# Optimization experiments

Measured on AMD Instinct MI355X. Metric: run time of the kernel, lower is better.

The kernel has to match this reference:

```python
import jax, jax.numpy as jnp
import numpy as np

DIM = 512
NUM_HEADS = 8
POS_DIM = 2
K_CLUSTERS = 256
M_PTS = 256


def setup_inputs() -> dict:
    key = jax.random.key(0)
    ks = jax.random.split(key, 9)
    pos = jax.random.uniform(ks[0], (K_CLUSTERS, M_PTS, POS_DIM), dtype=jnp.float32)
    feat = jax.random.normal(ks[1], (K_CLUSTERS, M_PTS, DIM), dtype=jnp.float32)
    mask = jax.random.randint(ks[2], (K_CLUSTERS, M_PTS, 1), 0, 2, dtype=jnp.int32)
    s = 0.02
    qkv_w = jax.random.normal(ks[3], (DIM, 3 * DIM), dtype=jnp.float32) * s
    qkv_b = jnp.zeros((3 * DIM,), dtype=jnp.float32)
    pos_w = jax.random.normal(ks[4], (POS_DIM, NUM_HEADS), dtype=jnp.float32) * s
    pos_b = jnp.zeros((NUM_HEADS,), dtype=jnp.float32)
    proj_w = jax.random.normal(ks[5], (DIM, DIM), dtype=jnp.float32) * s
    proj_b = jnp.zeros((DIM,), dtype=jnp.float32)
    return {"pos": pos, "feat": feat, "qkv_w": qkv_w, "qkv_b": qkv_b,
            "pos_w": pos_w, "pos_b": pos_b, "proj_w": proj_w, "proj_b": proj_b,
            "mask": mask}


def reference(pos, feat, qkv_w, qkv_b, pos_w, pos_b, proj_w, proj_b, mask):
    k_, m, c = feat.shape
    H = pos_w.shape[1]
    hd = c // H
    scale = hd ** -0.5

    # qkv projection -> (3, k, H, m, hd)
    qkv = (feat @ qkv_w + qkv_b).reshape(k_, m, 3, H, hd).transpose(2, 0, 3, 1, 4)
    q, k, v = qkv[0], qkv[1], qkv[2]

    attn = jnp.einsum('khid,khjd->khij', q * scale, k)  # k,H,m,m

    # normalize each coordinate by its global max over all clusters/points
    pos_n = pos / jnp.max(pos, axis=(0, 1), keepdims=True)
    # rel_pos[k,a,b,d] = pos[k,b,d] - pos[k,a,d]
    rel_pos = pos_n[:, None, :, :] - pos_n[:, :, None, :]  # k,m,m,d
    pos_bias = rel_pos @ pos_w + pos_b                      # k,m,m,H
    attn = attn + pos_bias.transpose(0, 3, 1, 2)            # k,H,m,m

    # mask: k,m,1 -> additive bias over key dim
    maskf = mask[:, :, 0].astype(attn.dtype)                # k,m
    attn = attn + ((1.0 - maskf) * -100.0)[:, None, None, :]

    attn = jax.nn.softmax(attn, axis=-1)
    x = jnp.einsum('khij,khjd->khid', attn, v)              # k,H,m,hd
    x = x.transpose(0, 2, 1, 3).reshape(k_, m, c)
    x = x @ proj_w + proj_b
    return x
```

## Files before the change

kernel.cpp:

```cpp
#include <hip/hip_runtime.h>
#include <stdint.h>

typedef short bf16x8 __attribute__((ext_vector_type(8)));
typedef float f32x4 __attribute__((ext_vector_type(4)));
typedef unsigned short u16x4 __attribute__((ext_vector_type(4)));
typedef unsigned short ushort_t;

__device__ __forceinline__ float bf2f(unsigned short u) {
    union { unsigned int i; float f; } v; v.i = ((unsigned int)u) << 16; return v.f;
}
__device__ __forceinline__ unsigned short f2bf(float f) {
    union { float f; unsigned int i; } v; v.f = f;
    unsigned int r = (v.i + 0x7FFFu + ((v.i >> 16) & 1u)) >> 16;
    return (unsigned short)r;
}

__device__ __forceinline__ void gload_lds16(const void* g, void* l) {
    __builtin_amdgcn_global_load_lds(
        (const __attribute__((address_space(1))) void*)g,
        (__attribute__((address_space(3))) void*)l, 16, 0, 0);
}

template <bool F32> struct LD;
template <> struct LD<false> {
    static __device__ __forceinline__ float s(const void* p, size_t i) {
        return bf2f(((const ushort_t*)p)[i]);
    }
    static __device__ __forceinline__ bf16x8 v8(const void* p, size_t i) {
        return *reinterpret_cast<const bf16x8*>((const ushort_t*)p + i);
    }
};
template <> struct LD<true> {
    static __device__ __forceinline__ float s(const void* p, size_t i) {
        return ((const float*)p)[i];
    }
    static __device__ __forceinline__ bf16x8 v8(const void* p, size_t i) {
        const float* f = (const float*)p + i;
        float4 a = *reinterpret_cast<const float4*>(f);
        float4 b = *reinterpret_cast<const float4*>(f + 4);
        bf16x8 r;
        r[0] = (short)f2bf(a.x); r[1] = (short)f2bf(a.y);
        r[2] = (short)f2bf(a.z); r[3] = (short)f2bf(a.w);
        r[4] = (short)f2bf(b.x); r[5] = (short)f2bf(b.y);
        r[6] = (short)f2bf(b.z); r[7] = (short)f2bf(b.w);
        return r;
    }
};

__global__ __launch_bounds__(64) void kprobe(const ushort_t* __restrict__ pos, int* __restrict__ dt) {
    float v = bf2f(pos[2 * threadIdx.x]);
    bool sane = (v >= 0.0f) && (v <= 1.0f);
    unsigned long long b = __ballot(sane);
    if (threadIdx.x == 0) dt[0] = (b == ~0ULL) ? 1 : 0;
}

template <bool F32>
static __device__ __forceinline__ void kpos_body(const void* pos, int* pmax, float* s0, float* s1) {
    int p = blockIdx.x * 256 + threadIdx.x;
    s0[threadIdx.x] = LD<F32>::s(pos, 2 * (size_t)p);
    s1[threadIdx.x] = LD<F32>::s(pos, 2 * (size_t)p + 1);
    __syncthreads();
    for (int off = 128; off > 0; off >>= 1) {
        if (threadIdx.x < (unsigned)off) {
            s0[threadIdx.x] = fmaxf(s0[threadIdx.x], s0[threadIdx.x + off]);
            s1[threadIdx.x] = fmaxf(s1[threadIdx.x], s1[threadIdx.x + off]);
        }
        __syncthreads();
    }
    if (threadIdx.x == 0) {
        atomicMax(&pmax[0], __float_as_int(s0[0]));
        atomicMax(&pmax[1], __float_as_int(s1[0]));
    }
}
__global__ __launch_bounds__(256) void kpos_max(const int* __restrict__ dt, const void* __restrict__ pos,
                                                int* __restrict__ pmax) {
    __shared__ float s0[256], s1[256];
    if (dt[0]) kpos_body<false>(pos, pmax, s0, s1);
    else       kpos_body<true>(pos, pmax, s0, s1);
}

template <bool F32>
static __device__ __forceinline__ void ktb_body(const void* pos, const void* pos_w, const int* mask,
                                                const int* pmax, float* tb) {
    int p = blockIdx.x * 256 + threadIdx.x;
    float inv0 = 1.0f / __int_as_float(pmax[0]);
    float inv1 = 1.0f / __int_as_float(pmax[1]);
    float x0 = LD<F32>::s(pos, 2 * (size_t)p) * inv0;
    float x1 = LD<F32>::s(pos, 2 * (size_t)p + 1) * inv1;
    float mterm = mask[p] ? 0.0f : -100.0f;
#pragma unroll
    for (int h = 0; h < 8; h++)
        tb[p * 8 + h] = x0 * LD<F32>::s(pos_w, h) + x1 * LD<F32>::s(pos_w, 8 + h) + mterm;
}
__global__ __launch_bounds__(256) void ktb(const int* __restrict__ dt, const void* __restrict__ pos,
                                           const void* __restrict__ pos_w, const int* __restrict__ mask,
                                           const int* __restrict__ pmax, float* __restrict__ tb) {
    if (dt[0]) ktb_body<false>(pos, pos_w, mask, pmax, tb);
    else       ktb_body<true>(pos, pos_w, mask, pmax, tb);
}

__global__ __launch_bounds__(256) void kbias(const int* __restrict__ dt, const void* __restrict__ qkv_b,
                                             const void* __restrict__ proj_b,
                                             float* __restrict__ qb, float* __restrict__ pb) {
    int i = blockIdx.x * 256 + threadIdx.x;
    if (dt[0]) {
        if (i < 1536) qb[i] = bf2f(((const ushort_t*)qkv_b)[i]);
        if (i < 512)  pb[i] = bf2f(((const ushort_t*)proj_b)[i]);
    } else {
        if (i < 1536) qb[i] = ((const float*)qkv_b)[i];
        if (i < 512)  pb[i] = ((const float*)proj_b)[i];
    }
}

template <bool F32>
static __device__ __forceinline__ void kfeat_body(const void* feat, ushort_t* featb) {
    for (size_t t = (size_t)blockIdx.x * 256 + threadIdx.x; t < 4194304; t += (size_t)gridDim.x * 256) {
        *reinterpret_cast<bf16x8*>(featb + t * 8) = LD<F32>::v8(feat, t * 8);
    }
}
__global__ __launch_bounds__(256) void kfeat(const int* __restrict__ dt, const void* __restrict__ feat,
                                             ushort_t* __restrict__ featb) {
    if (dt[0]) kfeat_body<false>(feat, featb);
    else       kfeat_body<true>(feat, featb);
}

template <bool F32>
static __device__ __forceinline__ void ktrans_body(const void* src, ushort_t* dst, int R, int C,
                                                   ushort_t* tile ) {
    int nbc = C >> 6;
    int rb = (blockIdx.x / nbc) << 6;
    int cb = (blockIdx.x % nbc) << 6;
    for (int i = threadIdx.x; i < 4096; i += 256) {
        int r = i >> 6, c = i & 63;
        tile[r * 65 + c] = f2bf(LD<F32>::s(src, (size_t)(rb + r) * C + cb + c));
    }
    __syncthreads();
    for (int i = threadIdx.x; i < 4096; i += 256) {
        int rr = i & 63, cc = i >> 6;
        dst[(size_t)(cb + cc) * R + rb + rr] = tile[rr * 65 + cc];
    }
}
__global__ __launch_bounds__(256) void ktrans(const int* __restrict__ dt, const void* __restrict__ src,
                                              ushort_t* __restrict__ dst, int R, int C) {
    __shared__ ushort_t tile[64 * 65];
    if (dt[0]) ktrans_body<false>(src, dst, R, C, tile);
    else       ktrans_body<true>(src, dst, R, C, tile);
}

template <bool F32>
static __device__ __forceinline__ void kattn_body(const void* feat, const ushort_t* qkv_wt,
                                                  const float* qb, const float* tb, ushort_t* xout,
                                                  ushort_t* smem) {
    const int tid = threadIdx.x;
    const int lane = tid & 63;
    const int wave = tid >> 6;
    const int quad = lane >> 4;
    const int l15 = lane & 15;

    const int bx = blockIdx.x;
    const int xcd = bx & 7;
    const int jj = bx >> 3;
    const int rr = jj >> 5;
    const int ss = jj & 31;
    const int kc = xcd * 32 + rr * 4 + (ss >> 3);
    const int h = ss & 7;

    ushort_t* sQ  = smem;
    ushort_t* sK  = smem + 18432;
    ushort_t* sVt = smem + 36864;
    ushort_t* sP  = smem + 53760;
    float*    stb = (float*)(smem + 72192);
    char*     stg = (char*)smem;

    if (tid < 256) stb[tid] = tb[(size_t)(kc * 256 + tid) * 8 + h];

    const int t0 = tid, t1 = tid + 512, t2 = tid + 1024;
    const int r0 = t0 >> 3, r1 = t1 >> 3, r2 = t2 >> 3;
    const ushort_t* g0 = qkv_wt + (size_t)((r0 >> 6) * 512 + h * 64 + (r0 & 63)) * 512 + (((t0 & 7) ^ (r0 & 7)) * 8);
    const ushort_t* g1 = qkv_wt + (size_t)((r1 >> 6) * 512 + h * 64 + (r1 & 63)) * 512 + (((t1 & 7) ^ (r1 & 7)) * 8);
    const ushort_t* g2 = qkv_wt + (size_t)((r2 >> 6) * 512 + h * 64 + (r2 & 63)) * 512 + (((t2 & 7) ^ (r2 & 7)) * 8);

    const int wrow = (wave >> 1) * 64;
    const int wcol = (wave & 1) * 96;

    f32x4 acc[4][6];
#pragma unroll
    for (int rt = 0; rt < 4; rt++)
#pragma unroll
        for (int ct = 0; ct < 6; ct++) {
            f32x4 z = {0.0f, 0.0f, 0.0f, 0.0f};
            acc[rt][ct] = z;
        }

    const size_t fbase = (size_t)(kc * 256) * 512;

    gload_lds16(g0, stg + t0 * 16);
    gload_lds16(g1, stg + t1 * 16);
    gload_lds16(g2, stg + t2 * 16);
    __syncthreads();

#pragma unroll 2
    for (int it = 0; it < 8; it++) {
        if (it < 7) {
            const int nb = ((it + 1) & 1) * 24576;
            gload_lds16(g0 + (it + 1) * 64, stg + nb + t0 * 16);
            gload_lds16(g1 + (it + 1) * 64, stg + nb + t1 * 16);
            gload_lds16(g2 + (it + 1) * 64, stg + nb + t2 * 16);
        }
        const int cbu = (it & 1) * 12288;
#pragma unroll
        for (int s = 0; s < 2; s++) {
            bf16x8 af[4];
#pragma unroll
            for (int rt = 0; rt < 4; rt++)
                af[rt] = LD<F32>::v8(
                    feat, fbase + (size_t)(wrow + rt * 16 + l15) * 512 + it * 64 + s * 32 + quad * 8);
            bf16x8 bw[6];
#pragma unroll
            for (int ct = 0; ct < 6; ct++) {
                const int rw = wcol + ct * 16 + l15;
                bw[ct] = *reinterpret_cast<const bf16x8*>(
                    smem + cbu + rw * 64 + (((s * 4 + quad) ^ (rw & 7)) * 8));
            }
#pragma unroll
            for (int ct = 0; ct < 6; ct++)
#pragma unroll
                for (int rt = 0; rt < 4; rt++)
                    acc[rt][ct] = __builtin_amdgcn_mfma_f32_16x16x32_bf16(af[rt], bw[ct], acc[rt][ct], 0, 0, 0);
        }
        __syncthreads();
    }

#pragma unroll
    for (int ct = 0; ct < 6; ct++) {
        const int lcb = wcol + ct * 16;
        const int mat = lcb >> 6;
        const int col = (lcb & 63) + l15;
        const float bias = qb[mat * 512 + h * 64 + col];
#pragma unroll
        for (int rt = 0; rt < 4; rt++) {
            const int m0 = wrow + rt * 16 + quad * 4;
            if (mat == 0) {
#pragma unroll
                for (int r = 0; r < 4; r++)
                    sQ[(m0 + r) * 72 + col] = f2bf((acc[rt][ct][r] + bias) * 0.125f);
            } else if (mat == 1) {
#pragma unroll
                for (int r = 0; r < 4; r++)
                    sK[(m0 + r) * 72 + col] = f2bf(acc[rt][ct][r] + bias);
            } else {
                u16x4 vp;
#pragma unroll
                for (int r = 0; r < 4; r++) vp[r] = f2bf(acc[rt][ct][r] + bias);
                *reinterpret_cast<u16x4*>(&sVt[col * 264 + m0]) = vp;
            }
        }
    }
    __syncthreads();

    bf16x8 aQ[2][2];
#pragma unroll
    for (int rt = 0; rt < 2; rt++)
#pragma unroll
        for (int s = 0; s < 2; s++)
            aQ[rt][s] = *reinterpret_cast<const bf16x8*>(
                &sQ[(wave * 32 + rt * 16 + l15) * 72 + s * 32 + quad * 8]);

    f32x4 accO[2][4];
    float rs[2][4];
#pragma unroll
    for (int rt = 0; rt < 2; rt++)
#pragma unroll
        for (int ct = 0; ct < 4; ct++) {
            f32x4 z = {0.0f, 0.0f, 0.0f, 0.0f};
            accO[rt][ct] = z;
            rs[rt][ct] = 0.0f;
        }

    ushort_t* sPw = sP + wave * (32 * 72);

    for (int jb = 0; jb < 4; jb++) {
        int kb = jb * 64;
        bf16x8 bK[4][2];
#pragma unroll
        for (int ctk = 0; ctk < 4; ctk++)
#pragma unroll
            for (int s = 0; s < 2; s++)
                bK[ctk][s] = *reinterpret_cast<const bf16x8*>(
                    &sK[(kb + ctk * 16 + l15) * 72 + s * 32 + quad * 8]);

#pragma unroll
        for (int ctk = 0; ctk < 4; ctk++) {
            float tcol = stb[kb + ctk * 16 + l15];
#pragma unroll
            for (int rt = 0; rt < 2; rt++) {
                f32x4 sa = {0.0f, 0.0f, 0.0f, 0.0f};
                sa = __builtin_amdgcn_mfma_f32_16x16x32_bf16(aQ[rt][0], bK[ctk][0], sa, 0, 0, 0);
                sa = __builtin_amdgcn_mfma_f32_16x16x32_bf16(aQ[rt][1], bK[ctk][1], sa, 0, 0, 0);
                int rl0 = rt * 16 + quad * 4;
#pragma unroll
                for (int r = 0; r < 4; r++) {
                    float pexp = __expf(sa[r] + tcol);
                    rs[rt][r] += pexp;
                    sPw[(rl0 + r) * 72 + ctk * 16 + l15] = f2bf(pexp);
                }
            }
        }

#pragma unroll
        for (int s = 0; s < 2; s++) {
            bf16x8 aP[2];
#pragma unroll
            for (int rt = 0; rt < 2; rt++)
                aP[rt] = *reinterpret_cast<const bf16x8*>(
                    &sPw[(rt * 16 + l15) * 72 + s * 32 + quad * 8]);
#pragma unroll
            for (int ct = 0; ct < 4; ct++) {
                bf16x8 bV = *reinterpret_cast<const bf16x8*>(
                    &sVt[(ct * 16 + l15) * 264 + kb + s * 32 + quad * 8]);
#pragma unroll
                for (int rt = 0; rt < 2; rt++)
                    accO[rt][ct] =
                        __builtin_amdgcn_mfma_f32_16x16x32_bf16(aP[rt], bV, accO[rt][ct], 0, 0, 0);
            }
        }
    }

    float inv_[2][4];
#pragma unroll
    for (int rt = 0; rt < 2; rt++)
#pragma unroll
        for (int r = 0; r < 4; r++) {
            float v = rs[rt][r];
            v += __shfl_xor(v, 1, 64);
            v += __shfl_xor(v, 2, 64);
            v += __shfl_xor(v, 4, 64);
            v += __shfl_xor(v, 8, 64);
            inv_[rt][r] = 1.0f / v;
        }

#pragma unroll
    for (int rt = 0; rt < 2; rt++)
#pragma unroll
        for (int ct = 0; ct < 4; ct++)
#pragma unroll
            for (int r = 0; r < 4; r++) {
                int m = wave * 32 + rt * 16 + quad * 4 + r;
                xout[((size_t)(kc * 256 + m)) * 512 + h * 64 + ct * 16 + l15] =
                    f2bf(accO[rt][ct][r] * inv_[rt][r]);
            }
}
__global__ __launch_bounds__(512, 2) void kattn_bf(const ushort_t* __restrict__ featb,
                                                   const ushort_t* __restrict__ qkv_wt,
                                                   const float* __restrict__ qb,
                                                   const float* __restrict__ tb, ushort_t* __restrict__ xout) {
    __shared__ ushort_t smem[72704];
    kattn_body<false>(featb, qkv_wt, qb, tb, xout, smem);
}
__global__ __launch_bounds__(512, 2) void kattn_dyn(const int* __restrict__ dt, const void* __restrict__ feat,
                                                    const ushort_t* __restrict__ qkv_wt,
                                                    const float* __restrict__ qb,
                                                    const float* __restrict__ tb, ushort_t* __restrict__ xout) {
    __shared__ ushort_t smem[72704];
    if (dt[0]) kattn_body<false>(feat, qkv_wt, qb, tb, xout, smem);
    else       kattn_body<true>(feat, qkv_wt, qb, tb, xout, smem);
}

template <bool F32>
static __device__ __forceinline__ void kproj_body(const ushort_t* x, const ushort_t* proj_wt,
                                                  const float* pb, void* out, ushort_t* sW) {
    const int tid = threadIdx.x;
    const int lane = tid & 63;
    const int wave = tid >> 6;
    const int quad = lane >> 4;
    const int l15 = lane & 15;
    const int bx = blockIdx.x;
    const int xcd = bx & 7;
    const int j = bx >> 3;
    const int rowb = (xcd * 32 + (j >> 2)) * 256;
    const int colb = (j & 3) * 128;
    const int rowg = (wave >> 1) * 64;
    const int colg = (wave & 1) * 64;
    char* stg = (char*)sW;

    const int t0 = tid, t1 = tid + 512;
    const int r0 = t0 >> 3, r1 = t1 >> 3;
    const ushort_t* g0 = proj_wt + (size_t)(colb + r0) * 512 + (((t0 & 7) ^ (r0 & 7)) * 8);
    const ushort_t* g1 = proj_wt + (size_t)(colb + r1) * 512 + (((t1 & 7) ^ (r1 & 7)) * 8);

    f32x4 acc[4][4];
#pragma unroll
    for (int rt = 0; rt < 4; rt++)
#pragma unroll
        for (int ct = 0; ct < 4; ct++) {
            f32x4 z = {0.0f, 0.0f, 0.0f, 0.0f};
            acc[rt][ct] = z;
        }

    gload_lds16(g0, stg + t0 * 16);
    gload_lds16(g1, stg + t1 * 16);
    __syncthreads();

#pragma unroll 2
    for (int it = 0; it < 8; it++) {
        if (it < 7) {
            const int nb = ((it + 1) & 1) * 16384;
            gload_lds16(g0 + (it + 1) * 64, stg + nb + t0 * 16);
            gload_lds16(g1 + (it + 1) * 64, stg + nb + t1 * 16);
        }
        const int cbu = (it & 1) * 8192;
#pragma unroll
        for (int s = 0; s < 2; s++) {
            bf16x8 af[4];
#pragma unroll
            for (int rt = 0; rt < 4; rt++) {
                int m = rowb + rowg + rt * 16 + l15;
                af[rt] = *reinterpret_cast<const bf16x8*>(
                    x + (size_t)m * 512 + it * 64 + s * 32 + quad * 8);
            }
            bf16x8 bw[4];
#pragma unroll
            for (int ct = 0; ct < 4; ct++) {
                const int rw = colg + ct * 16 + l15;
                bw[ct] = *reinterpret_cast<const bf16x8*>(
                    sW + cbu + rw * 64 + (((s * 4 + quad) ^ (rw & 7)) * 8));
            }
#pragma unroll
            for (int ct = 0; ct < 4; ct++)
#pragma unroll
                for (int rt = 0; rt < 4; rt++)
                    acc[rt][ct] = __builtin_amdgcn_mfma_f32_16x16x32_bf16(af[rt], bw[ct], acc[rt][ct], 0, 0, 0);
        }
        __syncthreads();
    }

#pragma unroll
    for (int ct = 0; ct < 4; ct++) {
        int n = colb + colg + ct * 16 + l15;
        float bias = pb[n];
#pragma unroll
        for (int rt = 0; rt < 4; rt++)
#pragma unroll
            for (int r = 0; r < 4; r++) {
                int m = rowb + rowg + rt * 16 + quad * 4 + r;
                float v = acc[rt][ct][r] + bias;
                if (F32) ((float*)out)[(size_t)m * 512 + n] = v;
                else     ((ushort_t*)out)[(size_t)m * 512 + n] = f2bf(v);
            }
    }
}
__global__ __launch_bounds__(512, 4) void kproj(const int* __restrict__ dt, const ushort_t* __restrict__ x,
                                                const ushort_t* __restrict__ proj_wt,
                                                const float* __restrict__ pb, void* __restrict__ out) {
    __shared__ ushort_t sW[16384];
    if (dt[0]) kproj_body<false>(x, proj_wt, pb, out, sW);
    else       kproj_body<true>(x, proj_wt, pb, out, sW);
}

extern "C" void kernel_launch(void* const* d_in, const int* in_sizes, int n_in,
                              void* d_out, int out_size, void* d_ws, size_t ws_size,
                              hipStream_t stream) {
    (void)in_sizes; (void)n_in; (void)out_size;
    const void* pos    = d_in[0];
    const void* feat   = d_in[1];
    const void* qkv_w  = d_in[2];
    const void* qkv_b  = d_in[3];
    const void* pos_w  = d_in[4];
    const void* proj_w = d_in[6];
    const void* proj_b = d_in[7];
    const int* mask    = (const int*)d_in[8];

    char* ws = (char*)d_ws;
    int* pmax         = (int*)ws;
    int* dtf          = (int*)ws + 2;
    float* qb         = (float*)(ws + 256);
    float* pb         = (float*)(ws + 256 + 6144);
    float* tb         = (float*)(ws + 16384);
    ushort_t* qkv_wt  = (ushort_t*)(ws + 16384 + 2097152);
    ushort_t* proj_wt = qkv_wt + 786432;
    ushort_t* x       = proj_wt + 262144;
    ushort_t* featb   = x + 33554432;
    const size_t NEED = 16384 + 2097152 + 1572864 + 524288 + 67108864 + 67108864;
    const bool big = ws_size >= NEED;

    (void)hipMemsetAsync(ws, 0, 16, stream);
    kprobe<<<1, 64, 0, stream>>>((const ushort_t*)pos, dtf);
    kpos_max<<<256, 256, 0, stream>>>(dtf, pos, pmax);
    ktb<<<256, 256, 0, stream>>>(dtf, pos, pos_w, mask, pmax, tb);
    kbias<<<6, 256, 0, stream>>>(dtf, qkv_b, proj_b, qb, pb);
    ktrans<<<192, 256, 0, stream>>>(dtf, qkv_w, qkv_wt, 512, 1536);
    ktrans<<<64, 256, 0, stream>>>(dtf, proj_w, proj_wt, 512, 512);
    if (big) {
        kfeat<<<2048, 256, 0, stream>>>(dtf, feat, featb);
        kattn_bf<<<2048, 512, 0, stream>>>(featb, qkv_wt, qb, tb, x);
    } else {
        kattn_dyn<<<2048, 512, 0, stream>>>(dtf, feat, qkv_wt, qb, tb, x);
    }
    kproj<<<1024, 512, 0, stream>>>(dtf, x, proj_wt, pb, d_out);
}
```

Before: 594.3 us.

## Merge preprocessing kernels into one launch and compute pos/mask bias inside attention

Replaces the probe, pos-max, bias, transpose and feature-conversion kernels with a single kprep kernel whose blocks are partitioned by index across those tasks. The per-point pos/mask bias table is no longer precomputed; the attention kernel now computes it from pos, pos_w, mask and the global max. The QKV weight staging in the attention GEMM changes from 64-wide swizzled chunks to 32-wide double-buffered chunks over 16 iterations, and LDS is split into separate arrays. This removes several launches and a workspace round trip, in exchange for more barriers per GEMM pass and possibly more LDS bank conflicts without the swizzle.

```diff
diff --git a/kernel.cpp b/kernel.cpp
--- a/kernel.cpp
+++ b/kernel.cpp
@@ -47,16 +47,26 @@
     }
 };
 
-__global__ __launch_bounds__(64) void kprobe(const ushort_t* __restrict__ pos, int* __restrict__ dt) {
-    float v = bf2f(pos[2 * threadIdx.x]);
-    bool sane = (v >= 0.0f) && (v <= 1.0f);
-    unsigned long long b = __ballot(sane);
-    if (threadIdx.x == 0) dt[0] = (b == ~0ULL) ? 1 : 0;
-}
-
 template <bool F32>
-static __device__ __forceinline__ void kpos_body(const void* pos, int* pmax, float* s0, float* s1) {
-    int p = blockIdx.x * 256 + threadIdx.x;
+static __device__ __forceinline__ void ktrans_body(const void* src, ushort_t* dst, int R, int C,
+                                                   ushort_t* tile , int bx) {
+    int nbc = C >> 6;
+    int rb = (bx / nbc) << 6;
+    int cb = (bx % nbc) << 6;
+    for (int i = threadIdx.x; i < 4096; i += 256) {
+        int r = i >> 6, c = i & 63;
+        tile[r * 65 + c] = f2bf(LD<F32>::s(src, (size_t)(rb + r) * C + cb + c));
+    }
+    __syncthreads();
+    for (int i = threadIdx.x; i < 4096; i += 256) {
+        int rr = i & 63, cc = i >> 6;
+        dst[(size_t)(cb + cc) * R + rb + rr] = tile[rr * 65 + cc];
+    }
+}
+
+template <bool F32>
+static __device__ __forceinline__ void kpos_body(const void* pos, int* pmax, float* s0, float* s1, int bx) {
+    int p = bx * 256 + threadIdx.x;
     s0[threadIdx.x] = LD<F32>::s(pos, 2 * (size_t)p);
     s1[threadIdx.x] = LD<F32>::s(pos, 2 * (size_t)p + 1);
     __syncthreads();
@@ -72,85 +82,72 @@
         atomicMax(&pmax[1], __float_as_int(s1[0]));
     }
 }
-__global__ __launch_bounds__(256) void kpos_max(const int* __restrict__ dt, const void* __restrict__ pos,
-                                                int* __restrict__ pmax) {
-    __shared__ float s0[256], s1[256];
-    if (dt[0]) kpos_body<false>(pos, pmax, s0, s1);
-    else       kpos_body<true>(pos, pmax, s0, s1);
-}
-
-template <bool F32>
-static __device__ __forceinline__ void ktb_body(const void* pos, const void* pos_w, const int* mask,
-                                                const int* pmax, float* tb) {
-    int p = blockIdx.x * 256 + threadIdx.x;
-    float inv0 = 1.0f / __int_as_float(pmax[0]);
-    float inv1 = 1.0f / __int_as_float(pmax[1]);
-    float x0 = LD<F32>::s(pos, 2 * (size_t)p) * inv0;
-    float x1 = LD<F32>::s(pos, 2 * (size_t)p + 1) * inv1;
-    float mterm = mask[p] ? 0.0f : -100.0f;
-#pragma unroll
-    for (int h = 0; h < 8; h++)
-        tb[p * 8 + h] = x0 * LD<F32>::s(pos_w, h) + x1 * LD<F32>::s(pos_w, 8 + h) + mterm;
-}
-__global__ __launch_bounds__(256) void ktb(const int* __restrict__ dt, const void* __restrict__ pos,
-                                           const void* __restrict__ pos_w, const int* __restrict__ mask,
-                                           const int* __restrict__ pmax, float* __restrict__ tb) {
-    if (dt[0]) ktb_body<false>(pos, pos_w, mask, pmax, tb);
-    else       ktb_body<true>(pos, pos_w, mask, pmax, tb);
-}
-
-__global__ __launch_bounds__(256) void kbias(const int* __restrict__ dt, const void* __restrict__ qkv_b,
-                                             const void* __restrict__ proj_b,
-                                             float* __restrict__ qb, float* __restrict__ pb) {
-    int i = blockIdx.x * 256 + threadIdx.x;
-    if (dt[0]) {
-        if (i < 1536) qb[i] = bf2f(((const ushort_t*)qkv_b)[i]);
-        if (i < 512)  pb[i] = bf2f(((const ushort_t*)proj_b)[i]);
+
+__global__ __launch_bounds__(256) void kprep(const void* __restrict__ pos, const void* __restrict__ feat,
+                                             const void* __restrict__ qkv_w, const void* __restrict__ proj_w,
+                                             const void* __restrict__ qkv_b, const void* __restrict__ proj_b,
+                                             int* __restrict__ pmax, int* __restrict__ dtf,
+                                             float* __restrict__ qb, float* __restrict__ pb,
+                                             ushort_t* __restrict__ featb,
+                                             ushort_t* __restrict__ qkv_wt, ushort_t* __restrict__ proj_wt) {
+    __shared__ char smem[8448];
+    __shared__ int sdt;
+    const int tid = threadIdx.x;
+    if (tid < 64) {
+        float v = bf2f(((const ushort_t*)pos)[2 * tid]);
+        bool sane = (v >= 0.0f) && (v <= 1.0f);
+        unsigned long long b = __ballot(sane);
+        if (tid == 0) sdt = (b == ~0ULL) ? 1 : 0;
+    }
+    __syncthreads();
+    const bool isbf = (sdt != 0);
+    const int bx = blockIdx.x;
+
+    if (bx < 192) {
+        ushort_t* tile = (ushort_t*)smem;
+        if (isbf) ktrans_body<false>(qkv_w, qkv_wt, 512, 1536, tile, bx);
+        else      ktrans_body<true>(qkv_w, qkv_wt, 512, 1536, tile, bx);
+    } else if (bx < 256) {
+        ushort_t* tile = (ushort_t*)smem;
+        if (isbf) ktrans_body<false>(proj_w, proj_wt, 512, 512, tile, bx - 192);
+        else      ktrans_body<true>(proj_w, proj_wt, 512, 512, tile, bx - 192);
+    } else if (bx < 512) {
+        float* s0 = (float*)smem;
+        float* s1 = s0 + 256;
+        if (isbf) kpos_body<false>(pos, pmax, s0, s1, bx - 256);
+        else      kpos_body<true>(pos, pmax, s0, s1, bx - 256);
+    } else if (bx == 512) {
+        if (tid == 0) dtf[0] = isbf ? 1 : 0;
+        for (int i = tid; i < 1536; i += 256)
+            qb[i] = isbf ? bf2f(((const ushort_t*)qkv_b)[i]) : ((const float*)qkv_b)[i];
+        for (int i = tid; i < 512; i += 256)
+            pb[i] = isbf ? bf2f(((const ushort_t*)proj_b)[i]) : ((const float*)proj_b)[i];
     } else {
-        if (i < 1536) qb[i] = ((const float*)qkv_b)[i];
-        if (i < 512)  pb[i] = ((const float*)proj_b)[i];
-    }
-}
-
-template <bool F32>
-static __device__ __forceinline__ void kfeat_body(const void* feat, ushort_t* featb) {
-    for (size_t t = (size_t)blockIdx.x * 256 + threadIdx.x; t < 4194304; t += (size_t)gridDim.x * 256) {
-        *reinterpret_cast<bf16x8*>(featb + t * 8) = LD<F32>::v8(feat, t * 8);
-    }
-}
-__global__ __launch_bounds__(256) void kfeat(const int* __restrict__ dt, const void* __restrict__ feat,
-                                             ushort_t* __restrict__ featb) {
-    if (dt[0]) kfeat_body<false>(feat, featb);
-    else       kfeat_body<true>(feat, featb);
-}
-
-template <bool F32>
-static __device__ __forceinline__ void ktrans_body(const void* src, ushort_t* dst, int R, int C,
-                                                   ushort_t* tile ) {
-    int nbc = C >> 6;
-    int rb = (blockIdx.x / nbc) << 6;
-    int cb = (blockIdx.x % nbc) << 6;
-    for (int i = threadIdx.x; i < 4096; i += 256) {
-        int r = i >> 6, c = i & 63;
-        tile[r * 65 + c] = f2bf(LD<F32>::s(src, (size_t)(rb + r) * C + cb + c));
-    }
-    __syncthreads();
-    for (int i = threadIdx.x; i < 4096; i += 256) {
-        int rr = i & 63, cc = i >> 6;
-        dst[(size_t)(cb + cc) * R + rb + rr] = tile[rr * 65 + cc];
-    }
-}
-__global__ __launch_bounds__(256) void ktrans(const int* __restrict__ dt, const void* __restrict__ src,
-                                              ushort_t* __restrict__ dst, int R, int C) {
-    __shared__ ushort_t tile[64 * 65];
-    if (dt[0]) ktrans_body<false>(src, dst, R, C, tile);
-    else       ktrans_body<true>(src, dst, R, C, tile);
+        const int fb = bx - 513;
+        if (isbf) {
+#pragma unroll
+            for (int i = 0; i < 8; i++) {
+                size_t t = (size_t)fb * 256 + tid + (size_t)i * 524288;
+                *reinterpret_cast<bf16x8*>(featb + t * 8) = LD<false>::v8(feat, t * 8);
+            }
+        } else {
+#pragma unroll
+            for (int i = 0; i < 8; i++) {
+                size_t t = (size_t)fb * 256 + tid + (size_t)i * 524288;
+                *reinterpret_cast<bf16x8*>(featb + t * 8) = LD<true>::v8(feat, t * 8);
+            }
+        }
+    }
 }
 
 template <bool F32>
 static __device__ __forceinline__ void kattn_body(const void* feat, const ushort_t* qkv_wt,
-                                                  const float* qb, const float* tb, ushort_t* xout,
-                                                  ushort_t* smem) {
+                                                  const float* qb,
+                                                  const void* pos, const void* pos_w,
+                                                  const int* mask, const int* pmax, int dtv,
+                                                  ushort_t* xout,
+                                                  ushort_t* sQ, ushort_t* sK, ushort_t* sVt,
+                                                  ushort_t* sP, float* stb) {
     const int tid = threadIdx.x;
     const int lane = tid & 63;
     const int wave = tid >> 6;
@@ -165,23 +162,41 @@
     const int kc = xcd * 32 + rr * 4 + (ss >> 3);
     const int h = ss & 7;
 
-    ushort_t* sQ  = smem;
-    ushort_t* sK  = smem + 18432;
-    ushort_t* sVt = smem + 36864;
-    ushort_t* sP  = smem + 53760;
-    float*    stb = (float*)(smem + 72192);
-    char*     stg = (char*)smem;
-
-    if (tid < 256) stb[tid] = tb[(size_t)(kc * 256 + tid) * 8 + h];
-
-    const int t0 = tid, t1 = tid + 512, t2 = tid + 1024;
-    const int r0 = t0 >> 3, r1 = t1 >> 3, r2 = t2 >> 3;
-    const ushort_t* g0 = qkv_wt + (size_t)((r0 >> 6) * 512 + h * 64 + (r0 & 63)) * 512 + (((t0 & 7) ^ (r0 & 7)) * 8);
-    const ushort_t* g1 = qkv_wt + (size_t)((r1 >> 6) * 512 + h * 64 + (r1 & 63)) * 512 + (((t1 & 7) ^ (r1 & 7)) * 8);
-    const ushort_t* g2 = qkv_wt + (size_t)((r2 >> 6) * 512 + h * 64 + (r2 & 63)) * 512 + (((t2 & 7) ^ (r2 & 7)) * 8);
+    if (tid < 256) {
+        const int p = kc * 256 + tid;
+        const float inv0 = 1.0f / __int_as_float(pmax[0]);
+        const float inv1 = 1.0f / __int_as_float(pmax[1]);
+        float x0, x1, w0, w1;
+        if (dtv) {
+            x0 = bf2f(((const ushort_t*)pos)[2 * (size_t)p]);
+            x1 = bf2f(((const ushort_t*)pos)[2 * (size_t)p + 1]);
+            w0 = bf2f(((const ushort_t*)pos_w)[h]);
+            w1 = bf2f(((const ushort_t*)pos_w)[8 + h]);
+        } else {
+            x0 = ((const float*)pos)[2 * (size_t)p];
+            x1 = ((const float*)pos)[2 * (size_t)p + 1];
+            w0 = ((const float*)pos_w)[h];
+            w1 = ((const float*)pos_w)[8 + h];
+        }
+        x0 *= inv0;
+        x1 *= inv1;
+        const float mterm = mask[p] ? 0.0f : -100.0f;
+        stb[tid] = x0 * w0 + x1 * w1 + mterm;
+    }
+
+    ushort_t* sW = sP;
+    char* ldsW = (char*)sW;
+
+    const int t1 = wave * 64 + lane;
+    const int t2 = 512 + t1;
+    const int lc1 = t1 >> 2, ch1 = t1 & 3;
+    const int lc2 = t2 >> 2, ch2 = t2 & 3;
+    const ushort_t* g1 = qkv_wt + (size_t)((lc1 >> 6) * 512 + h * 64 + (lc1 & 63)) * 512 + ch1 * 8;
+    const ushort_t* g2 = qkv_wt + (size_t)((lc2 >> 6) * 512 + h * 64 + (lc2 & 63)) * 512 + ch2 * 8;
 
     const int wrow = (wave >> 1) * 64;
     const int wcol = (wave & 1) * 96;
+    const int fcol = quad * 8;
 
     f32x4 acc[4][6];
 #pragma unroll
@@ -194,40 +209,31 @@
 
     const size_t fbase = (size_t)(kc * 256) * 512;
 
-    gload_lds16(g0, stg + t0 * 16);
-    gload_lds16(g1, stg + t1 * 16);
-    gload_lds16(g2, stg + t2 * 16);
+    gload_lds16(g1, ldsW + wave * 1024);
+    if (wave < 4) gload_lds16(g2, ldsW + 8192 + wave * 1024);
     __syncthreads();
 
 #pragma unroll 2
-    for (int it = 0; it < 8; it++) {
-        if (it < 7) {
-            const int nb = ((it + 1) & 1) * 24576;
-            gload_lds16(g0 + (it + 1) * 64, stg + nb + t0 * 16);
-            gload_lds16(g1 + (it + 1) * 64, stg + nb + t1 * 16);
-            gload_lds16(g2 + (it + 1) * 64, stg + nb + t2 * 16);
-        }
-        const int cbu = (it & 1) * 12288;
-#pragma unroll
-        for (int s = 0; s < 2; s++) {
-            bf16x8 af[4];
+    for (int c = 0; c < 16; c++) {
+        const int cb = (c & 1) * 6144;
+        const int nbB = ((c + 1) & 1) * 12288;
+        if (c < 15) {
+            gload_lds16(g1 + (c + 1) * 32, ldsW + nbB + wave * 1024);
+            if (wave < 4) gload_lds16(g2 + (c + 1) * 32, ldsW + nbB + 8192 + wave * 1024);
+        }
+        bf16x8 af[4];
+#pragma unroll
+        for (int rt = 0; rt < 4; rt++)
+            af[rt] = LD<F32>::v8(feat, fbase + (size_t)(wrow + rt * 16 + l15) * 512 + c * 32 + fcol);
+        bf16x8 bw[6];
+#pragma unroll
+        for (int ct = 0; ct < 6; ct++)
+            bw[ct] = *reinterpret_cast<const bf16x8*>(sW + cb + (wcol + ct * 16 + l15) * 32 + fcol);
+#pragma unroll
+        for (int ct = 0; ct < 6; ct++)
 #pragma unroll
             for (int rt = 0; rt < 4; rt++)
-                af[rt] = LD<F32>::v8(
-                    feat, fbase + (size_t)(wrow + rt * 16 + l15) * 512 + it * 64 + s * 32 + quad * 8);
-            bf16x8 bw[6];
-#pragma unroll
-            for (int ct = 0; ct < 6; ct++) {
-                const int rw = wcol + ct * 16 + l15;
-                bw[ct] = *reinterpret_cast<const bf16x8*>(
-                    smem + cbu + rw * 64 + (((s * 4 + quad) ^ (rw & 7)) * 8));
-            }
-#pragma unroll
-            for (int ct = 0; ct < 6; ct++)
-#pragma unroll
-                for (int rt = 0; rt < 4; rt++)
-                    acc[rt][ct] = __builtin_amdgcn_mfma_f32_16x16x32_bf16(af[rt], bw[ct], acc[rt][ct], 0, 0, 0);
-        }
+                acc[rt][ct] = __builtin_amdgcn_mfma_f32_16x16x32_bf16(af[rt], bw[ct], acc[rt][ct], 0, 0, 0);
         __syncthreads();
     }
 
@@ -353,17 +359,34 @@
 __global__ __launch_bounds__(512, 2) void kattn_bf(const ushort_t* __restrict__ featb,
                                                    const ushort_t* __restrict__ qkv_wt,
                                                    const float* __restrict__ qb,
-                                                   const float* __restrict__ tb, ushort_t* __restrict__ xout) {
-    __shared__ ushort_t smem[72704];
-    kattn_body<false>(featb, qkv_wt, qb, tb, xout, smem);
-}
-__global__ __launch_bounds__(512, 2) void kattn_dyn(const int* __restrict__ dt, const void* __restrict__ feat,
+                                                   const void* __restrict__ pos,
+                                                   const void* __restrict__ pos_w,
+                                                   const int* __restrict__ mask,
+                                                   const int* __restrict__ pmax,
+                                                   const int* __restrict__ dtf,
+                                                   ushort_t* __restrict__ xout) {
+    __shared__ ushort_t sQ[256 * 72];
+    __shared__ ushort_t sK[256 * 72];
+    __shared__ ushort_t sVt[64 * 264];
+    __shared__ ushort_t sP[8 * 32 * 72];
+    __shared__ float stb[256];
+    kattn_body<false>(featb, qkv_wt, qb, pos, pos_w, mask, pmax, dtf[0], xout, sQ, sK, sVt, sP, stb);
+}
+__global__ __launch_bounds__(512, 2) void kattn_dyn(const int* __restrict__ dtf, const void* __restrict__ feat,
                                                     const ushort_t* __restrict__ qkv_wt,
                                                     const float* __restrict__ qb,
-                                                    const float* __restrict__ tb, ushort_t* __restrict__ xout) {
-    __shared__ ushort_t smem[72704];
-    if (dt[0]) kattn_body<false>(feat, qkv_wt, qb, tb, xout, smem);
-    else       kattn_body<true>(feat, qkv_wt, qb, tb, xout, smem);
+                                                    const void* __restrict__ pos,
+                                                    const void* __restrict__ pos_w,
+                                                    const int* __restrict__ mask,
+                                                    const int* __restrict__ pmax,
+                                                    ushort_t* __restrict__ xout) {
+    __shared__ ushort_t sQ[256 * 72];
+    __shared__ ushort_t sK[256 * 72];
+    __shared__ ushort_t sVt[64 * 264];
+    __shared__ ushort_t sP[8 * 32 * 72];
+    __shared__ float stb[256];
+    if (dtf[0]) kattn_body<false>(feat, qkv_wt, qb, pos, pos_w, mask, pmax, 1, xout, sQ, sK, sVt, sP, stb);
+    else        kattn_body<true>(feat, qkv_wt, qb, pos, pos_w, mask, pmax, 0, xout, sQ, sK, sVt, sP, stb);
 }
 
 template <bool F32>
@@ -475,26 +498,20 @@
     int* dtf          = (int*)ws + 2;
     float* qb         = (float*)(ws + 256);
     float* pb         = (float*)(ws + 256 + 6144);
-    float* tb         = (float*)(ws + 16384);
-    ushort_t* qkv_wt  = (ushort_t*)(ws + 16384 + 2097152);
+    ushort_t* qkv_wt  = (ushort_t*)(ws + 16384);
     ushort_t* proj_wt = qkv_wt + 786432;
     ushort_t* x       = proj_wt + 262144;
     ushort_t* featb   = x + 33554432;
-    const size_t NEED = 16384 + 2097152 + 1572864 + 524288 + 67108864 + 67108864;
+    const size_t NEED = 16384 + 1572864 + 524288 + 67108864 + 67108864;
     const bool big = ws_size >= NEED;
 
     (void)hipMemsetAsync(ws, 0, 16, stream);
-    kprobe<<<1, 64, 0, stream>>>((const ushort_t*)pos, dtf);
-    kpos_max<<<256, 256, 0, stream>>>(dtf, pos, pmax);
-    ktb<<<256, 256, 0, stream>>>(dtf, pos, pos_w, mask, pmax, tb);
-    kbias<<<6, 256, 0, stream>>>(dtf, qkv_b, proj_b, qb, pb);
-    ktrans<<<192, 256, 0, stream>>>(dtf, qkv_w, qkv_wt, 512, 1536);
-    ktrans<<<64, 256, 0, stream>>>(dtf, proj_w, proj_wt, 512, 512);
+    kprep<<<big ? 2561 : 513, 256, 0, stream>>>(pos, feat, qkv_w, proj_w, qkv_b, proj_b,
+                                                pmax, dtf, qb, pb, featb, qkv_wt, proj_wt);
     if (big) {
-        kfeat<<<2048, 256, 0, stream>>>(dtf, feat, featb);
-        kattn_bf<<<2048, 512, 0, stream>>>(featb, qkv_wt, qb, tb, x);
+        kattn_bf<<<2048, 512, 0, stream>>>(featb, qkv_wt, qb, pos, pos_w, mask, pmax, dtf, x);
     } else {
-        kattn_dyn<<<2048, 512, 0, stream>>>(dtf, feat, qkv_wt, qb, tb, x);
+        kattn_dyn<<<2048, 512, 0, stream>>>(dtf, feat, qkv_wt, qb, pos, pos_w, mask, pmax, x);
     }
     kproj<<<1024, 512, 0, stream>>>(dtf, x, proj_wt, pb, d_out);
 }
```

Measured after the change: 557.2 us. 1.07x faster.
